# Kernel tuning notes

Hardware: AMD Instinct MI355X
Metric: run time of the kernel (lower is better)

## Reference

```python
import jax, jax.numpy as jnp
import numpy as np

N_EDGES = 65536
D = 512          # n_hidden
H = 8            # num_heads
DH = D // H      # head_dim
LN_EPS = 1e-5


def _layernorm(x, g, b):
    m = jnp.mean(x, axis=-1, keepdims=True)
    v = jnp.mean(jnp.square(x - m), axis=-1, keepdims=True)
    return (x - m) * jax.lax.rsqrt(v + LN_EPS) * g + b


def setup_inputs() -> dict:
    key = jax.random.key(0)
    ks = jax.random.split(key, 10)
    s = 1.0 / np.sqrt(D)      # ~kaiming-uniform scale for nn.Linear
    s4 = 1.0 / np.sqrt(4 * D)
    return {
        "query_input": jax.random.normal(ks[0], (N_EDGES, D), jnp.float32),
        "source_input": jax.random.normal(ks[1], (N_EDGES, D), jnp.float32),
        "Wq": jax.random.normal(ks[2], (D, D), jnp.float32) * s,
        "bq": jnp.zeros((D,), jnp.float32),
        "Wk": jax.random.normal(ks[3], (D, D), jnp.float32) * s,
        "bk": jnp.zeros((D,), jnp.float32),
        "Wv": jax.random.normal(ks[4], (D, D), jnp.float32) * s,
        "bv": jnp.zeros((D,), jnp.float32),
        "Wh": jax.random.normal(ks[5], (D, D), jnp.float32) * s,
        "bh": jnp.zeros((D,), jnp.float32),
        "ln_kv_g": jnp.ones((D,), jnp.float32),
        "ln_kv_b": jnp.zeros((D,), jnp.float32),
        "ln_q_g": jnp.ones((D,), jnp.float32),
        "ln_q_b": jnp.zeros((D,), jnp.float32),
        "ln2_g": jnp.ones((D,), jnp.float32),
        "ln2_b": jnp.zeros((D,), jnp.float32),
        "W1": jax.random.normal(ks[6], (D, 4 * D), jnp.float32) * s,
        "b1": jnp.zeros((4 * D,), jnp.float32),
        "W2": jax.random.normal(ks[7], (4 * D, D), jnp.float32) * s4,
        "b2": jnp.zeros((D,), jnp.float32),
    }


def reference(query_input, source_input, Wq, bq, Wk, bk, Wv, bv, Wh, bh,
              ln_kv_g, ln_kv_b, ln_q_g, ln_q_b, ln2_g, ln2_b,
              W1, b1, W2, b2):
    n = query_input.shape[0]
    ln_src = _layernorm(source_input, ln_kv_g, ln_kv_b)
    ln_qry = _layernorm(query_input, ln_q_g, ln_q_b)

    qs = (ln_qry @ Wq + bq).reshape(n, H, DH)
    ks = (ln_src @ Wk + bk).reshape(n, H, DH)
    vs = (ln_src @ Wv + bv).reshape(n, H, DH)

    # torch.norm(qs, p=2) with no dim => GLOBAL Frobenius norm (faithful to source)
    qs = qs / jnp.linalg.norm(qs)
    ks = ks / jnp.linalg.norm(ks)

    nf = jnp.asarray(n, qs.dtype)
    kvs = jnp.einsum('nhd,nhk->hdk', ks, vs)                 # [H, DH, DH]
    # 'nhd,hdd->nhd' : repeated d on kvs takes its DIAGONAL (torch semantics)
    attention_num = jnp.einsum('nhd,hdd->nhd', qs, kvs) + vs * nf
    ks_sum = jnp.sum(ks, axis=0)                             # == einsum('nhd,n->hd', ks, ones)
    normalizer = jnp.einsum('nhd,hd->nh', qs, ks_sum)[..., None] + nf
    attn_output = (attention_num / normalizer).reshape(n, H * DH)

    h_post_attention = attn_output @ Wh + bh
    h_pre_ffn = source_input + h_post_attention              # dropout = identity (eval)
    y = _layernorm(h_pre_ffn, ln2_g, ln2_b)
    h_post_ffn = jax.nn.gelu(y @ W1 + b1, approximate=False) @ W2 + b2
    return h_pre_ffn + h_post_ffn
```

## Files before the change

kernel.cpp:

```cpp
#include <hip/hip_runtime.h>
#include <hip/hip_bf16.h>

#define NROWS 65536
#define LN_EPS 1e-5f

typedef __attribute__((ext_vector_type(8))) short bf16x8;
typedef __attribute__((ext_vector_type(4))) float f32x4;

__device__ __forceinline__ float bf2f(unsigned short u) {
  union { unsigned u; float f; } c; c.u = ((unsigned)u) << 16; return c.f;
}
__device__ __forceinline__ unsigned short f2bf(float f) {
  union { float f; unsigned u; } c; c.f = f;
  return (unsigned short)((c.u + 0x7fffu + ((c.u >> 16) & 1u)) >> 16);
}

__launch_bounds__(256)
__global__ void normcast_k(const float* __restrict__ x, unsigned short* __restrict__ o) {
  int t = threadIdx.x;
  int row = blockIdx.x * 4 + (t >> 6);
  int lane = t & 63;
  const float* p = x + (size_t)row * 512 + lane * 8;
  float4 a = *(const float4*)p;
  float4 b = *(const float4*)(p + 4);
  float s = a.x + a.y + a.z + a.w + b.x + b.y + b.z + b.w;
  float q = a.x*a.x + a.y*a.y + a.z*a.z + a.w*a.w
          + b.x*b.x + b.y*b.y + b.z*b.z + b.w*b.w;
#pragma unroll
  for (int off = 1; off < 64; off <<= 1) {
    s += __shfl_xor(s, off);
    q += __shfl_xor(q, off);
  }
  float mean = s * (1.0f / 512.0f);
  float r = rsqrtf(q * (1.0f / 512.0f) - mean * mean + LN_EPS);
  float va[8] = {a.x, a.y, a.z, a.w, b.x, b.y, b.z, b.w};
  unsigned pk[4];
#pragma unroll
  for (int i = 0; i < 4; ++i) {
    unsigned lo = f2bf((va[2 * i] - mean) * r);
    unsigned hi = f2bf((va[2 * i + 1] - mean) * r);
    pk[i] = lo | (hi << 16);
  }
  uint4 u; u.x = pk[0]; u.y = pk[1]; u.z = pk[2]; u.w = pk[3];
  *(uint4*)(o + (size_t)row * 512 + lane * 8) = u;
}

__launch_bounds__(256)
__global__ void transbf_k(const float* __restrict__ W, const float* __restrict__ g,
                          unsigned short* __restrict__ Wt, int K, int N) {
  __shared__ float tile[32][33];
  int tx = threadIdx.x & 31, ty = threadIdx.x >> 5;
  int n0 = blockIdx.x * 32, k0 = blockIdx.y * 32;
#pragma unroll
  for (int i = 0; i < 4; ++i) {
    int k = k0 + ty + i * 8;
    float gg = g ? g[k] : 1.0f;
    tile[ty + i * 8][tx] = gg * W[(size_t)k * N + n0 + tx];
  }
  __syncthreads();
#pragma unroll
  for (int i = 0; i < 4; ++i) {
    int n = n0 + ty + i * 8;
    Wt[(size_t)n * K + k0 + tx] = f2bf(tile[tx][ty + i * 8]);
  }
}

__launch_bounds__(256)
__global__ void betacalc_k(const float* __restrict__ W, const float* __restrict__ b,
                           const float* __restrict__ bias, float* __restrict__ beta,
                           int K, int N) {
  int n = blockIdx.x * 256 + threadIdx.x;
  float s = 0.f;
  for (int k = 0; k < K; ++k) s += b[k] * W[(size_t)k * N + n];
  beta[n] = s + bias[n];
}

#define M_Q  0
#define M_K  1
#define M_V  2
#define M_H  3
#define M_F1 4
#define M_F2 5

template <int MODE>
__launch_bounds__(256)
__global__ void mm_k(const unsigned short* __restrict__ A,
                     const unsigned short* __restrict__ Bt,
                     void* __restrict__ Ov,
                     const float* __restrict__ beta,
                     const float* __restrict__ src,
                     float* __restrict__ scal,
                     int N, int K) {
  __shared__ __align__(16) unsigned short As[128 * 64];
  __shared__ __align__(16) unsigned short Bs[128 * 64];
  __shared__ float red[4];
  const int t = threadIdx.x;
  const int lane = t & 63;
  const int wave = t >> 6;

  const unsigned gx = gridDim.x;
  unsigned bid = blockIdx.y * gx + blockIdx.x;
  const unsigned cpx = (gx * gridDim.y) >> 3;
  bid = (bid & 7u) * cpx + (bid >> 3);
  const int m0 = (int)(bid / gx) * 128;
  const int n0 = (int)(bid % gx) * 128;

  const int srow = lane >> 3;
  const int sxor = ((lane & 7) ^ srow) * 8;
  const int wm = (wave >> 1) * 64;
  const int wn = (wave & 1) * 64;
  const int quad = lane >> 4;
  const int l15 = lane & 15;
  const int l7 = lane & 7;

  f32x4 acc[4][4];
#pragma unroll
  for (int i = 0; i < 4; ++i)
#pragma unroll
    for (int j = 0; j < 4; ++j) acc[i][j] = (f32x4){0.f, 0.f, 0.f, 0.f};

  for (int k0 = 0; k0 < K; k0 += 64) {
    __syncthreads();
#pragma unroll
    for (int i = 0; i < 4; ++i) {
      int c = wave * 4 + i;
      int grow = c * 8 + srow;
      const unsigned short* ga = A + (size_t)(m0 + grow) * K + k0 + sxor;
      const unsigned short* gb = Bt + (size_t)(n0 + grow) * K + k0 + sxor;
      __builtin_amdgcn_global_load_lds(
          (const __attribute__((address_space(1))) void*)ga,
          (__attribute__((address_space(3))) void*)(As + c * 512), 16, 0, 0);
      __builtin_amdgcn_global_load_lds(
          (const __attribute__((address_space(1))) void*)gb,
          (__attribute__((address_space(3))) void*)(Bs + c * 512), 16, 0, 0);
    }
    __syncthreads();
#pragma unroll
    for (int kt = 0; kt < 2; ++kt) {
      const int pb = ((kt * 4 + quad) ^ l7) * 8;
      bf16x8 af[4], bfr[4];
#pragma unroll
      for (int x = 0; x < 4; ++x) {
        af[x]  = *(const bf16x8*)(As + (wm + x * 16 + l15) * 64 + pb);
        bfr[x] = *(const bf16x8*)(Bs + (wn + x * 16 + l15) * 64 + pb);
      }
#pragma unroll
      for (int mi = 0; mi < 4; ++mi)
#pragma unroll
        for (int nj = 0; nj < 4; ++nj)
          acc[mi][nj] = __builtin_amdgcn_mfma_f32_16x16x32_bf16(
              af[mi], bfr[nj], acc[mi][nj], 0, 0, 0);
    }
  }

  float lred = 0.f;
#pragma unroll
  for (int mi = 0; mi < 4; ++mi) {
#pragma unroll
    for (int nj = 0; nj < 4; ++nj) {
      const int col = n0 + wn + nj * 16 + l15;
      const float bet = beta[col];
#pragma unroll
      for (int r = 0; r < 4; ++r) {
        const int row = m0 + wm + mi * 16 + quad * 4 + r;
        const size_t idx = (size_t)row * N + col;
        float v = acc[mi][nj][r] + bet;
        if constexpr (MODE == M_Q || MODE == M_K) {
          lred += v * v;
          ((unsigned short*)Ov)[idx] = f2bf(v);
        } else if constexpr (MODE == M_V) {
          ((unsigned short*)Ov)[idx] = f2bf(v);
        } else if constexpr (MODE == M_H) {
          ((float*)Ov)[idx] = v + src[idx];
        } else if constexpr (MODE == M_F1) {
          float gl = 0.5f * v * (1.0f + erff(v * 0.70710678118654752f));
          ((unsigned short*)Ov)[idx] = f2bf(gl);
        } else {
          ((float*)Ov)[idx] += v;
        }
      }
    }
  }
  if constexpr (MODE == M_Q || MODE == M_K) {
#pragma unroll
    for (int off = 32; off > 0; off >>= 1) lred += __shfl_xor(lred, off);
    if (lane == 0) red[wave] = lred;
    __syncthreads();
    if (t == 0) atomicAdd(scal, red[0] + red[1] + red[2] + red[3]);
  }
}

__launch_bounds__(256)
__global__ void colred_k(const unsigned short* __restrict__ Kb,
                         const unsigned short* __restrict__ Vb,
                         float* __restrict__ S1, float* __restrict__ S2) {
  int t = threadIdx.x;
  int c0 = t * 2;
  int r0 = blockIdx.x * 128;
  float s1a = 0.f, s1b = 0.f, s2a = 0.f, s2b = 0.f;
  for (int r = 0; r < 128; ++r) {
    unsigned ku = *(const unsigned*)(Kb + (size_t)(r0 + r) * 512 + c0);
    unsigned vu = *(const unsigned*)(Vb + (size_t)(r0 + r) * 512 + c0);
    float k0 = bf2f((unsigned short)(ku & 0xffff));
    float k1 = bf2f((unsigned short)(ku >> 16));
    float v0 = bf2f((unsigned short)(vu & 0xffff));
    float v1 = bf2f((unsigned short)(vu >> 16));
    s1a += k0 * v0; s1b += k1 * v1;
    s2a += k0;      s2b += k1;
  }
  atomicAdd(&S1[c0], s1a); atomicAdd(&S1[c0 + 1], s1b);
  atomicAdd(&S2[c0], s2a); atomicAdd(&S2[c0 + 1], s2b);
}

__launch_bounds__(256)
__global__ void attn_k(unsigned short* __restrict__ Qb, const unsigned short* __restrict__ Vb,
                       const float* __restrict__ S1, const float* __restrict__ S2,
                       const float* __restrict__ sqq, const float* __restrict__ skk) {
  int t = threadIdx.x;
  int row = blockIdx.x * 4 + (t >> 6);
  int lane = t & 63;
  int c = lane * 8;
  float inv = rsqrtf(sqq[0] * skk[0]);
  const float Nf = (float)NROWS;
  unsigned short* qp = Qb + (size_t)row * 512 + c;
  uint4 qu = *(const uint4*)qp;
  float q[8];
  q[0] = bf2f((unsigned short)(qu.x & 0xffff)); q[1] = bf2f((unsigned short)(qu.x >> 16));
  q[2] = bf2f((unsigned short)(qu.y & 0xffff)); q[3] = bf2f((unsigned short)(qu.y >> 16));
  q[4] = bf2f((unsigned short)(qu.z & 0xffff)); q[5] = bf2f((unsigned short)(qu.z >> 16));
  q[6] = bf2f((unsigned short)(qu.w & 0xffff)); q[7] = bf2f((unsigned short)(qu.w >> 16));
  const unsigned short* vp = Vb + (size_t)row * 512 + c;
  uint4 vu = *(const uint4*)vp;
  float vv[8];
  vv[0] = bf2f((unsigned short)(vu.x & 0xffff)); vv[1] = bf2f((unsigned short)(vu.x >> 16));
  vv[2] = bf2f((unsigned short)(vu.y & 0xffff)); vv[3] = bf2f((unsigned short)(vu.y >> 16));
  vv[4] = bf2f((unsigned short)(vu.z & 0xffff)); vv[5] = bf2f((unsigned short)(vu.z >> 16));
  vv[6] = bf2f((unsigned short)(vu.w & 0xffff)); vv[7] = bf2f((unsigned short)(vu.w >> 16));
  float4 s10 = *(const float4*)(S1 + c), s11 = *(const float4*)(S1 + c + 4);
  float4 s20 = *(const float4*)(S2 + c), s21 = *(const float4*)(S2 + c + 4);
  float s1v[8] = {s10.x, s10.y, s10.z, s10.w, s11.x, s11.y, s11.z, s11.w};
  float s2v[8] = {s20.x, s20.y, s20.z, s20.w, s21.x, s21.y, s21.z, s21.w};
  float part = 0.f;
#pragma unroll
  for (int i = 0; i < 8; ++i) part += q[i] * s2v[i];
  part += __shfl_xor(part, 1);
  part += __shfl_xor(part, 2);
  part += __shfl_xor(part, 4);
  float rn = 1.0f / (inv * part + Nf);
  unsigned pk[4];
#pragma unroll
  for (int i = 0; i < 4; ++i) {
    float o0 = (q[2 * i] * s1v[2 * i] * inv + vv[2 * i] * Nf) * rn;
    float o1 = (q[2 * i + 1] * s1v[2 * i + 1] * inv + vv[2 * i + 1] * Nf) * rn;
    pk[i] = (unsigned)f2bf(o0) | ((unsigned)f2bf(o1) << 16);
  }
  uint4 u; u.x = pk[0]; u.y = pk[1]; u.z = pk[2]; u.w = pk[3];
  *(uint4*)qp = u;
}

extern "C" void kernel_launch(void* const* d_in, const int* in_sizes, int n_in,
                              void* d_out, int out_size, void* d_ws, size_t ws_size,
                              hipStream_t stream) {
  const float* query   = (const float*)d_in[0];
  const float* source  = (const float*)d_in[1];
  const float* Wq      = (const float*)d_in[2];
  const float* bq      = (const float*)d_in[3];
  const float* Wk      = (const float*)d_in[4];
  const float* bk      = (const float*)d_in[5];
  const float* Wv      = (const float*)d_in[6];
  const float* bv      = (const float*)d_in[7];
  const float* Wh      = (const float*)d_in[8];
  const float* bh      = (const float*)d_in[9];
  const float* ln_kv_g = (const float*)d_in[10];
  const float* ln_kv_b = (const float*)d_in[11];
  const float* ln_q_g  = (const float*)d_in[12];
  const float* ln_q_b  = (const float*)d_in[13];
  const float* ln2_g   = (const float*)d_in[14];
  const float* ln2_b   = (const float*)d_in[15];
  const float* W1      = (const float*)d_in[16];
  const float* b1      = (const float*)d_in[17];
  const float* W2      = (const float*)d_in[18];
  const float* b2      = (const float*)d_in[19];
  float* out = (float*)d_out;

  const size_t MB = 1024 * 1024;
  char* w = (char*)d_ws;
  unsigned short* Qn = (unsigned short*)(w + 0 * MB);
  unsigned short* Sn = (unsigned short*)(w + 64 * MB);
  unsigned short* Qb = (unsigned short*)(w + 128 * MB);
  unsigned short* Kb = (unsigned short*)(w + 192 * MB);
  unsigned short* Vb = (unsigned short*)(w + 256 * MB);
  unsigned short* Hn = (unsigned short*)(w + 320 * MB);
  unsigned short* Tb = (unsigned short*)(w + 0 * MB);
  char* wt = w + 384 * MB;
  unsigned short* Wqt = (unsigned short*)wt;
  unsigned short* Wkt = Wqt + 512 * 512;
  unsigned short* Wvt = Wkt + 512 * 512;
  unsigned short* Wht = Wvt + 512 * 512;
  unsigned short* W1t = Wht + 512 * 512;
  unsigned short* W2t = W1t + 512 * 2048;
  float* betaq = (float*)(W2t + 2048 * 512);
  float* betak = betaq + 512;
  float* betav = betak + 512;
  float* betaf = betav + 512;
  float* S1 = betaf + 2048;
  float* S2 = S1 + 512;
  float* SQQ = S2 + 512;
  float* SKK = SQQ + 1;

  hipMemsetAsync(S1, 0, (512 + 512 + 2) * sizeof(float), stream);

  dim3 blk(256);
  normcast_k<<<NROWS / 4, blk, 0, stream>>>(query, Qn);
  normcast_k<<<NROWS / 4, blk, 0, stream>>>(source, Sn);
  transbf_k<<<dim3(16, 16), blk, 0, stream>>>(Wq, ln_q_g, Wqt, 512, 512);
  transbf_k<<<dim3(16, 16), blk, 0, stream>>>(Wk, ln_kv_g, Wkt, 512, 512);
  transbf_k<<<dim3(16, 16), blk, 0, stream>>>(Wv, ln_kv_g, Wvt, 512, 512);
  transbf_k<<<dim3(16, 16), blk, 0, stream>>>(Wh, nullptr, Wht, 512, 512);
  transbf_k<<<dim3(64, 16), blk, 0, stream>>>(W1, ln2_g, W1t, 512, 2048);
  transbf_k<<<dim3(16, 64), blk, 0, stream>>>(W2, nullptr, W2t, 2048, 512);
  betacalc_k<<<2, blk, 0, stream>>>(Wq, ln_q_b, bq, betaq, 512, 512);
  betacalc_k<<<2, blk, 0, stream>>>(Wk, ln_kv_b, bk, betak, 512, 512);
  betacalc_k<<<2, blk, 0, stream>>>(Wv, ln_kv_b, bv, betav, 512, 512);
  betacalc_k<<<8, blk, 0, stream>>>(W1, ln2_b, b1, betaf, 512, 2048);

  dim3 g512(4, 512);
  mm_k<M_Q><<<g512, blk, 0, stream>>>(Qn, Wqt, Qb, betaq, nullptr, SQQ, 512, 512);
  mm_k<M_K><<<g512, blk, 0, stream>>>(Sn, Wkt, Kb, betak, nullptr, SKK, 512, 512);
  mm_k<M_V><<<g512, blk, 0, stream>>>(Sn, Wvt, Vb, betav, nullptr, nullptr, 512, 512);
  colred_k<<<NROWS / 128, blk, 0, stream>>>(Kb, Vb, S1, S2);
  attn_k<<<NROWS / 4, blk, 0, stream>>>(Qb, Vb, S1, S2, SQQ, SKK);
  mm_k<M_H><<<g512, blk, 0, stream>>>(Qb, Wht, out, bh, source, nullptr, 512, 512);
  normcast_k<<<NROWS / 4, blk, 0, stream>>>(out, Hn);
  dim3 g2048(16, 512);
  mm_k<M_F1><<<g2048, blk, 0, stream>>>(Hn, W1t, Tb, betaf, nullptr, nullptr, 2048, 512);
  mm_k<M_F2><<<g512, blk, 0, stream>>>(Tb, W2t, out, b2, nullptr, nullptr, 512, 2048);
}
```

Before: 1.789 ms.

## Fuse K and V projections into one GEMM and use tanh-form GELU

Merges the separate K and V projection GEMMs into a single N=1024 GEMM that writes an interleaved KV buffer. It relies on the transposed Wk/Wv weights and their bias vectors already being contiguous, so the shared source activations are streamed once instead of twice. The colred and attn kernels are updated to read K and V from the combined row layout, and the squared-norm reduction only runs for the K half of the output. Separately, the FFN1 epilogue replaces the exact erf GELU with the tanh approximation computed via exp and a fast reciprocal, which slightly changes numerics relative to the exact-GELU reference.

```diff
diff --git a/kernel.cpp b/kernel.cpp
--- a/kernel.cpp
+++ b/kernel.cpp
@@ -76,8 +76,7 @@
 }
 
 #define M_Q  0
-#define M_K  1
-#define M_V  2
+#define M_KV 1
 #define M_H  3
 #define M_F1 4
 #define M_F2 5
@@ -160,20 +159,21 @@
     for (int nj = 0; nj < 4; ++nj) {
       const int col = n0 + wn + nj * 16 + l15;
       const float bet = beta[col];
-#pragma unroll
-      for (int r = 0; r < 4; ++r) {
-        const int row = m0 + wm + mi * 16 + quad * 4 + r;
-        const size_t idx = (size_t)row * N + col;
+      size_t idx = (size_t)(m0 + wm + mi * 16 + quad * 4) * N + col;
+#pragma unroll
+      for (int r = 0; r < 4; ++r, idx += N) {
         float v = acc[mi][nj][r] + bet;
-        if constexpr (MODE == M_Q || MODE == M_K) {
+        if constexpr (MODE == M_Q || MODE == M_KV) {
           lred += v * v;
-          ((unsigned short*)Ov)[idx] = f2bf(v);
-        } else if constexpr (MODE == M_V) {
           ((unsigned short*)Ov)[idx] = f2bf(v);
         } else if constexpr (MODE == M_H) {
           ((float*)Ov)[idx] = v + src[idx];
         } else if constexpr (MODE == M_F1) {
-          float gl = 0.5f * v * (1.0f + erff(v * 0.70710678118654752f));
+          float t2 = v * v;
+          float y2 = 1.5957691216f * v * __builtin_fmaf(0.044715f, t2, 1.0f);
+          float e = __expf(y2);
+          float rr = __builtin_amdgcn_rcpf(e + 1.0f);
+          float gl = v - v * rr;
           ((unsigned short*)Ov)[idx] = f2bf(gl);
         } else {
           ((float*)Ov)[idx] += v;
@@ -181,26 +181,28 @@
       }
     }
   }
-  if constexpr (MODE == M_Q || MODE == M_K) {
-#pragma unroll
-    for (int off = 32; off > 0; off >>= 1) lred += __shfl_xor(lred, off);
-    if (lane == 0) red[wave] = lred;
-    __syncthreads();
-    if (t == 0) atomicAdd(scal, red[0] + red[1] + red[2] + red[3]);
-  }
-}
-
-__launch_bounds__(256)
-__global__ void colred_k(const unsigned short* __restrict__ Kb,
-                         const unsigned short* __restrict__ Vb,
+  if constexpr (MODE == M_Q || MODE == M_KV) {
+    if (MODE == M_Q || n0 < 512) {
+#pragma unroll
+      for (int off = 32; off > 0; off >>= 1) lred += __shfl_xor(lred, off);
+      if (lane == 0) red[wave] = lred;
+      __syncthreads();
+      if (t == 0) atomicAdd(scal, red[0] + red[1] + red[2] + red[3]);
+    }
+  }
+}
+
+__launch_bounds__(256)
+__global__ void colred_k(const unsigned short* __restrict__ KV,
                          float* __restrict__ S1, float* __restrict__ S2) {
   int t = threadIdx.x;
   int c0 = t * 2;
   int r0 = blockIdx.x * 128;
   float s1a = 0.f, s1b = 0.f, s2a = 0.f, s2b = 0.f;
   for (int r = 0; r < 128; ++r) {
-    unsigned ku = *(const unsigned*)(Kb + (size_t)(r0 + r) * 512 + c0);
-    unsigned vu = *(const unsigned*)(Vb + (size_t)(r0 + r) * 512 + c0);
+    const unsigned short* base = KV + (size_t)(r0 + r) * 1024;
+    unsigned ku = *(const unsigned*)(base + c0);
+    unsigned vu = *(const unsigned*)(base + 512 + c0);
     float k0 = bf2f((unsigned short)(ku & 0xffff));
     float k1 = bf2f((unsigned short)(ku >> 16));
     float v0 = bf2f((unsigned short)(vu & 0xffff));
@@ -213,7 +215,7 @@
 }
 
 __launch_bounds__(256)
-__global__ void attn_k(unsigned short* __restrict__ Qb, const unsigned short* __restrict__ Vb,
+__global__ void attn_k(unsigned short* __restrict__ Qb, const unsigned short* __restrict__ KV,
                        const float* __restrict__ S1, const float* __restrict__ S2,
                        const float* __restrict__ sqq, const float* __restrict__ skk) {
   int t = threadIdx.x;
@@ -229,7 +231,7 @@
   q[2] = bf2f((unsigned short)(qu.y & 0xffff)); q[3] = bf2f((unsigned short)(qu.y >> 16));
   q[4] = bf2f((unsigned short)(qu.z & 0xffff)); q[5] = bf2f((unsigned short)(qu.z >> 16));
   q[6] = bf2f((unsigned short)(qu.w & 0xffff)); q[7] = bf2f((unsigned short)(qu.w >> 16));
-  const unsigned short* vp = Vb + (size_t)row * 512 + c;
+  const unsigned short* vp = KV + (size_t)row * 1024 + 512 + c;
   uint4 vu = *(const uint4*)vp;
   float vv[8];
   vv[0] = bf2f((unsigned short)(vu.x & 0xffff)); vv[1] = bf2f((unsigned short)(vu.x >> 16));
@@ -288,8 +290,7 @@
   unsigned short* Qn = (unsigned short*)(w + 0 * MB);
   unsigned short* Sn = (unsigned short*)(w + 64 * MB);
   unsigned short* Qb = (unsigned short*)(w + 128 * MB);
-  unsigned short* Kb = (unsigned short*)(w + 192 * MB);
-  unsigned short* Vb = (unsigned short*)(w + 256 * MB);
+  unsigned short* KV = (unsigned short*)(w + 192 * MB);
   unsigned short* Hn = (unsigned short*)(w + 320 * MB);
   unsigned short* Tb = (unsigned short*)(w + 0 * MB);
   char* wt = w + 384 * MB;
@@ -326,10 +327,9 @@
 
   dim3 g512(4, 512);
   mm_k<M_Q><<<g512, blk, 0, stream>>>(Qn, Wqt, Qb, betaq, nullptr, SQQ, 512, 512);
-  mm_k<M_K><<<g512, blk, 0, stream>>>(Sn, Wkt, Kb, betak, nullptr, SKK, 512, 512);
-  mm_k<M_V><<<g512, blk, 0, stream>>>(Sn, Wvt, Vb, betav, nullptr, nullptr, 512, 512);
-  colred_k<<<NROWS / 128, blk, 0, stream>>>(Kb, Vb, S1, S2);
-  attn_k<<<NROWS / 4, blk, 0, stream>>>(Qb, Vb, S1, S2, SQQ, SKK);
+  mm_k<M_KV><<<dim3(8, 512), blk, 0, stream>>>(Sn, Wkt, KV, betak, nullptr, SKK, 1024, 512);
+  colred_k<<<NROWS / 128, blk, 0, stream>>>(KV, S1, S2);
+  attn_k<<<NROWS / 4, blk, 0, stream>>>(Qb, KV, S1, S2, SQQ, SKK);
   mm_k<M_H><<<g512, blk, 0, stream>>>(Qb, Wht, out, bh, source, nullptr, 512, 512);
   normcast_k<<<NROWS / 4, blk, 0, stream>>>(out, Hn);
   dim3 g2048(16, 512);
```

New measurement: 1.770 ms. Within noise of the previous version (-1.1%).
